# Optimization experiments

Hardware: AMD Instinct MI355X
Metric: run time of the kernel (lower is better)

## Reference

```python
import jax, jax.numpy as jnp
import numpy as np

NEAR_THRESHOLD = 0.25
N = 1536          # entities (== max_entities)
D = 768           # d_model
H = 64            # classifier hidden width
NTYPES = 4        # relation types: 0=NEAR, 1=APPROACHING, 2=FLEEING, 3=ABOVE
SPATIAL = 8       # geometric feature dim


def setup_inputs() -> dict:
    key = jax.random.key(0)
    ks = jax.random.split(key, 6)
    entity_embeddings = jax.random.normal(ks[0], (N, D), dtype=jnp.float32)
    positions = jax.random.uniform(ks[1], (N, 3), dtype=jnp.float32)
    prev_positions = jax.random.uniform(ks[2], (N, 3), dtype=jnp.float32)
    in_dim = 2 * D + SPATIAL
    W1 = jax.random.normal(ks[3], (in_dim, H), dtype=jnp.float32) * (1.0 / np.sqrt(in_dim))
    b1 = jnp.zeros((H,), dtype=jnp.float32)
    W2 = jax.random.normal(ks[4], (H, NTYPES), dtype=jnp.float32) * (1.0 / np.sqrt(H))
    b2 = jnp.zeros((NTYPES,), dtype=jnp.float32)
    return {"entity_embeddings": entity_embeddings, "positions": positions,
            "prev_positions": prev_positions, "W1": W1, "b1": b1, "W2": W2, "b2": b2}


def reference(entity_embeddings, positions, prev_positions, W1, b1, W2, b2):
    n, d = entity_embeddings.shape
    velocities = positions - prev_positions
    # pairwise geometry: entry [i, j] corresponds to pair (a=i, b=j)
    rel_pos = positions[None, :, :] - positions[:, None, :]      # (N, N, 3) = pos_b - pos_a
    rel_vel = velocities[None, :, :] - velocities[:, None, :]    # (N, N, 3)
    distance = jnp.linalg.norm(rel_pos, axis=-1)                 # (N, N)
    closing = -(rel_pos * rel_vel).sum(-1) / jnp.maximum(distance, 1e-6)
    vdiff = rel_pos[..., 1]
    # spatial feats = [dx, dy, dz, dist, dvx, dvy, dvz, vertical_diff]
    sp = jnp.concatenate([rel_pos, distance[..., None], rel_vel, vdiff[..., None]], axis=-1)  # (N, N, 8)

    # first Linear on concat([emb_a, emb_b, sp]) decomposed into three projections
    W1a, W1b, W1s = W1[:d], W1[d:2 * d], W1[2 * d:]
    ha = entity_embeddings @ W1a                                  # (N, H)
    hb = entity_embeddings @ W1b                                  # (N, H)
    hidden = jax.nn.relu(ha[:, None, :] + hb[None, :, :]
                         + jnp.einsum('ijs,sh->ijh', sp, W1s) + b1)  # (N, N, H)
    logits = hidden @ W2 + b2                                     # (N, N, 4)
    probs = jax.nn.softmax(logits, axis=-1)
    best_idx = jnp.argmax(probs, axis=-1)
    conf = jnp.max(probs, axis=-1)

    # conditional overrides (same priority order as _classify_pair)
    near = distance < NEAR_THRESHOLD
    appr = ~near & (closing > 0.05)
    flee = ~near & ~appr & (closing < -0.05)
    above = ~near & ~appr & ~flee & (jnp.abs(vdiff) > 0.3) & (distance < 0.5)
    rel_type = jnp.where(near, 0,
               jnp.where(appr, 1,
               jnp.where(flee, 2,
               jnp.where(above, 3, best_idx)))).astype(jnp.int32)
    conf_out = jnp.where(near, jnp.maximum(conf, 0.8),
               jnp.where(appr, jnp.maximum(conf, 0.6),
               jnp.where(flee, jnp.maximum(conf, 0.6),
               jnp.where(above, jnp.maximum(conf, 0.5), conf))))

    upper = jnp.triu(jnp.ones((n, n), dtype=bool), k=1)           # i < j pairs only
    valid = upper & (conf_out > 0.3)
    return rel_type, conf_out, valid
```

## Files before the change

kernel.cpp:

```cpp
#include <hip/hip_runtime.h>

typedef float f4 __attribute__((ext_vector_type(4)));

#define N 1536
#define D 768
#define H 64
#define NN (N * N)

__global__ __launch_bounds__(128) void k1_gemm(
    const float* __restrict__ E, const float* __restrict__ pos,
    const float* __restrict__ ppos, const float* __restrict__ W1,
    const float* __restrict__ b1, float* __restrict__ P, int KC)
{
    __shared__ float Es[8][192];

    const int tid = threadIdx.x;
    const int i0  = blockIdx.x * 8;
    const int kcc = blockIdx.y;
    const int k0  = kcc * KC;

    const int hg  = tid & 31;
    const int h0  = hg * 4;
    const int mat = h0 >> 6;
    const int hc  = h0 & 63;
    const int rp  = tid >> 5;
    const float* Wbase = W1 + (size_t)(mat * D + k0) * H + hc;

    f4 acc0 = {0.f, 0.f, 0.f, 0.f};
    f4 acc1 = {0.f, 0.f, 0.f, 0.f};

    for (int ks = 0; ks < KC; ks += 192) {
        if (ks) __syncthreads();
        for (int f = tid; f < 8 * 48; f += 128) {
            int row = f / 48, c = f - row * 48;
            *(f4*)&Es[row][c * 4] =
                *(const f4*)&E[(size_t)(i0 + row) * D + k0 + ks + c * 4];
        }
        __syncthreads();

        const float* Wc  = Wbase + (size_t)ks * H;
        const float* e0p = Es[2 * rp];
        const float* e1p = Es[2 * rp + 1];
        for (int kk = 0; kk < 192; kk += 8) {
#pragma unroll
            for (int u = 0; u < 8; ++u) {
                f4 w = *(const f4*)&Wc[(size_t)(kk + u) * H];
                float e0 = e0p[kk + u], e1 = e1p[kk + u];
                acc0 = __builtin_elementwise_fma((f4){e0, e0, e0, e0}, w, acc0);
                acc1 = __builtin_elementwise_fma((f4){e1, e1, e1, e1}, w, acc1);
            }
        }
    }

    if (kcc == 0) {
        const float* Ws = W1 + (size_t)2 * D * H + hc;
        f4 wp0 = *(const f4*)&Ws[0 * H];
        f4 wp1 = *(const f4*)&Ws[1 * H] + *(const f4*)&Ws[7 * H];
        f4 wp2 = *(const f4*)&Ws[2 * H];
        f4 wv0 = *(const f4*)&Ws[4 * H];
        f4 wv1 = *(const f4*)&Ws[5 * H];
        f4 wv2 = *(const f4*)&Ws[6 * H];
        f4 bb  = *(const f4*)&b1[hc];
#pragma unroll
        for (int r = 0; r < 2; ++r) {
            int i = i0 + 2 * rp + r;
            float px = pos[3 * i], py = pos[3 * i + 1], pz = pos[3 * i + 2];
            float vx = px - ppos[3 * i];
            float vy = py - ppos[3 * i + 1];
            float vz = pz - ppos[3 * i + 2];
            f4 g = px * wp0 + py * wp1 + pz * wp2 + vx * wv0 + vy * wv1 + vz * wv2;
            f4 add = (mat == 0) ? (bb - g) : g;
            if (r == 0) acc0 += add; else acc1 += add;
        }
    }

#pragma unroll
    for (int r = 0; r < 2; ++r) {
        int i = i0 + 2 * rp + r;
        f4 a = r ? acc1 : acc0;
#pragma unroll
        for (int c = 0; c < 4; ++c)
            P[(size_t)(kcc * 128 + h0 + c) * N + i] = a[c];
    }
}

__global__ __launch_bounds__(128) void k2_main(
    const float* __restrict__ P, int nkc,
    const float* __restrict__ W1, const float* __restrict__ W2,
    const float* __restrict__ b2, const float* __restrict__ pos,
    const float* __restrict__ ppos, float* __restrict__ out)
{
    __shared__ float As[64][32];
    __shared__ f4 Bs[64][16];
    __shared__ float w3s[64];
    __shared__ f4 W2s[64];
    __shared__ float pis[32][3], vis[32][3], pjs[64][3], vjs[64][3];

    const int tid = threadIdx.x;
    const int i0 = blockIdx.y * 32;
    const int j0 = blockIdx.x * 64;

#pragma unroll
    for (int g = 0; g < 4; ++g) {
        int f = g * 128 + tid;
        int h = f >> 3, c = f & 7;
        f4 s = {0.f, 0.f, 0.f, 0.f};
        for (int kc = 0; kc < nkc; ++kc)
            s += *(const f4*)&P[(size_t)(kc * 128 + h) * N + i0 + c * 4];
        *(f4*)&As[h][c * 4] = s;
    }
#pragma unroll
    for (int g = 0; g < 8; ++g) {
        int f = g * 128 + tid;
        int h = f >> 4, c = f & 15;
        f4 s = {0.f, 0.f, 0.f, 0.f};
        for (int kc = 0; kc < nkc; ++kc)
            s += *(const f4*)&P[(size_t)(kc * 128 + 64 + h) * N + j0 + c * 4];
        Bs[h][c] = s;
    }
    if (tid < 64) {
        w3s[tid] = W1[(size_t)(2 * D + 3) * H + tid];
        W2s[tid] = *(const f4*)&W2[tid * 4];
        int j = j0 + tid;
        float px = pos[3 * j], py = pos[3 * j + 1], pz = pos[3 * j + 2];
        pjs[tid][0] = px; pjs[tid][1] = py; pjs[tid][2] = pz;
        vjs[tid][0] = px - ppos[3 * j];
        vjs[tid][1] = py - ppos[3 * j + 1];
        vjs[tid][2] = pz - ppos[3 * j + 2];
    } else if (tid < 96) {
        int t = tid - 64;
        int i = i0 + t;
        float px = pos[3 * i], py = pos[3 * i + 1], pz = pos[3 * i + 2];
        pis[t][0] = px; pis[t][1] = py; pis[t][2] = pz;
        vis[t][0] = px - ppos[3 * i];
        vis[t][1] = py - ppos[3 * i + 1];
        vis[t][2] = pz - ppos[3 * i + 2];
    }
    __syncthreads();

    const int tx = tid & 15;
    const int ty = tid >> 4;

    float dist[4][4];
    {
#pragma clang fp contract(off)
#pragma unroll
        for (int a = 0; a < 4; ++a) {
#pragma unroll
            for (int b = 0; b < 4; ++b) {
                int il = ty * 4 + a, jl = tx * 4 + b;
                float dx = pjs[jl][0] - pis[il][0];
                float dy = pjs[jl][1] - pis[il][1];
                float dz = pjs[jl][2] - pis[il][2];
                float s = dx * dx;
                s = s + dy * dy;
                s = s + dz * dz;
                dist[a][b] = sqrtf(s);
            }
        }
    }

    f4 acc[4][4];
#pragma unroll
    for (int a = 0; a < 4; ++a)
#pragma unroll
        for (int b = 0; b < 4; ++b)
            acc[a][b] = (f4){0.f, 0.f, 0.f, 0.f};

#pragma unroll 4
    for (int h = 0; h < 64; ++h) {
        f4 A4 = *(const f4*)&As[h][ty * 4];
        f4 B4 = Bs[h][tx];
        float w3h = w3s[h];
        f4 w2r = W2s[h];
#pragma unroll
        for (int a = 0; a < 4; ++a) {
#pragma unroll
            for (int b = 0; b < 4; ++b) {
                float hid = fmaf(dist[a][b], w3h, A4[a] + B4[b]);
                hid = fmaxf(hid, 0.f);
                acc[a][b] = __builtin_elementwise_fma(
                    (f4){hid, hid, hid, hid}, w2r, acc[a][b]);
            }
        }
    }

    const f4 B2v = *(const f4*)b2;

#pragma unroll
    for (int a = 0; a < 4; ++a) {
        int il = ty * 4 + a;
        int i = i0 + il;
        f4 rt4, cf4, vl4;
#pragma unroll
        for (int b = 0; b < 4; ++b) {
            int jl = tx * 4 + b;
            int j = j0 + jl;
            float dd = dist[a][b];
            float dy, closing;
            {
#pragma clang fp contract(off)
                float dx = pjs[jl][0] - pis[il][0];
                dy       = pjs[jl][1] - pis[il][1];
                float dz = pjs[jl][2] - pis[il][2];
                float rvx = vjs[jl][0] - vis[il][0];
                float rvy = vjs[jl][1] - vis[il][1];
                float rvz = vjs[jl][2] - vis[il][2];
                float dot = dx * rvx;
                dot = dot + dy * rvy;
                dot = dot + dz * rvz;
                closing = -dot / fmaxf(dd, 1e-6f);
            }
            f4 l = acc[a][b] + B2v;
            float mx = l.x; int bidx = 0;
            if (l.y > mx) { mx = l.y; bidx = 1; }
            if (l.z > mx) { mx = l.z; bidx = 2; }
            if (l.w > mx) { mx = l.w; bidx = 3; }
            float s = expf(l.x - mx);
            s += expf(l.y - mx);
            s += expf(l.z - mx);
            s += expf(l.w - mx);
            float conf = 1.0f / s;

            bool near = dd < 0.25f;
            bool appr = !near && (closing > 0.05f);
            bool flee = !near && !appr && (closing < -0.05f);
            bool above = !near && !appr && !flee && (fabsf(dy) > 0.3f) && (dd < 0.5f);
            int rt = near ? 0 : appr ? 1 : flee ? 2 : above ? 3 : bidx;
            float co = near  ? fmaxf(conf, 0.8f)
                     : appr  ? fmaxf(conf, 0.6f)
                     : flee  ? fmaxf(conf, 0.6f)
                     : above ? fmaxf(conf, 0.5f)
                             : conf;
            float vd = ((j > i) && (co > 0.3f)) ? 1.0f : 0.0f;
            rt4[b] = (float)rt;
            cf4[b] = co;
            vl4[b] = vd;
        }
        int col = j0 + tx * 4;
        *(f4*)&out[(size_t)i * N + col]                  = rt4;
        *(f4*)&out[(size_t)NN + (size_t)i * N + col]     = cf4;
        *(f4*)&out[(size_t)2 * NN + (size_t)i * N + col] = vl4;
    }
}

extern "C" void kernel_launch(void* const* d_in, const int* in_sizes, int n_in,
                              void* d_out, int out_size, void* d_ws, size_t ws_size,
                              hipStream_t stream)
{
    const float* E    = (const float*)d_in[0];
    const float* pos  = (const float*)d_in[1];
    const float* ppos = (const float*)d_in[2];
    const float* W1   = (const float*)d_in[3];
    const float* b1   = (const float*)d_in[4];
    const float* W2   = (const float*)d_in[5];
    const float* b2   = (const float*)d_in[6];
    float* out = (float*)d_out;
    float* P   = (float*)d_ws;

    int nkc = (ws_size >= (size_t)4 * 128 * N * 4) ? 4 : 1;
    int KC  = D / nkc;

    dim3 g1(N / 8, nkc);
    k1_gemm<<<g1, 128, 0, stream>>>(E, pos, ppos, W1, b1, P, KC);

    dim3 g2(N / 64, N / 32);
    k2_main<<<g2, 128, 0, stream>>>(P, nkc, W1, W2, b2, pos, ppos, out);
}
```

Measured before the change: 150.3 us.

## Shrink pair tile to 32x32, pre-reduce K-split partials, packed f2 math

Adds a separate reduce kernel that sums the K-split partial projections once, so the main kernel no longer re-reads and sums the partials in every tile. The main kernel tile drops from 32x64 to 32x32 pairs per block, giving twice as many blocks and fewer accumulators per thread. Geometry (distance, dy, closing) is now computed up front and kept in registers, and shared memory for geometry and projections is overlaid with a union. The hidden-layer loop uses 2-wide packed FMA/max and reads W2 and w3 straight from global memory instead of shared. The cost is an extra launch, more workspace, and less reuse per block.

```diff
diff --git a/kernel.cpp b/kernel.cpp
--- a/kernel.cpp
+++ b/kernel.cpp
@@ -1,6 +1,7 @@
 #include <hip/hip_runtime.h>
 
 typedef float f4 __attribute__((ext_vector_type(4)));
+typedef float f2 __attribute__((ext_vector_type(2)));
 
 #define N 1536
 #define D 768
@@ -84,104 +85,114 @@
     }
 }
 
+__global__ __launch_bounds__(256) void k1b_reduce(
+    const float* __restrict__ P, float* __restrict__ AB, int nkc)
+{
+    int idx = blockIdx.x * 256 + threadIdx.x;
+    f4 s = {0.f, 0.f, 0.f, 0.f};
+    for (int kc = 0; kc < nkc; ++kc)
+        s += *(const f4*)&P[(size_t)kc * 128 * N + (size_t)idx * 4];
+    *(f4*)&AB[(size_t)idx * 4] = s;
+}
+
 __global__ __launch_bounds__(128) void k2_main(
-    const float* __restrict__ P, int nkc,
-    const float* __restrict__ W1, const float* __restrict__ W2,
-    const float* __restrict__ b2, const float* __restrict__ pos,
-    const float* __restrict__ ppos, float* __restrict__ out)
-{
-    __shared__ float As[64][32];
-    __shared__ f4 Bs[64][16];
-    __shared__ float w3s[64];
-    __shared__ f4 W2s[64];
-    __shared__ float pis[32][3], vis[32][3], pjs[64][3], vjs[64][3];
+    const float* __restrict__ AB, const float* __restrict__ W1,
+    const float* __restrict__ W2, const float* __restrict__ b2,
+    const float* __restrict__ pos, const float* __restrict__ ppos,
+    float* __restrict__ out)
+{
+    __shared__ union SMem {
+        struct { float pi[32][3], vi[32][3], pj[32][3], vj[32][3]; } g;
+        struct { float As[64][32], Bs[64][32]; } t;
+    } sm;
 
     const int tid = threadIdx.x;
     const int i0 = blockIdx.y * 32;
-    const int j0 = blockIdx.x * 64;
+    const int j0 = blockIdx.x * 32;
+
+    if (tid < 32) {
+        int i = i0 + tid;
+        float px = pos[3 * i], py = pos[3 * i + 1], pz = pos[3 * i + 2];
+        sm.g.pi[tid][0] = px; sm.g.pi[tid][1] = py; sm.g.pi[tid][2] = pz;
+        sm.g.vi[tid][0] = px - ppos[3 * i];
+        sm.g.vi[tid][1] = py - ppos[3 * i + 1];
+        sm.g.vi[tid][2] = pz - ppos[3 * i + 2];
+    } else if (tid < 64) {
+        int t = tid - 32;
+        int j = j0 + t;
+        float px = pos[3 * j], py = pos[3 * j + 1], pz = pos[3 * j + 2];
+        sm.g.pj[t][0] = px; sm.g.pj[t][1] = py; sm.g.pj[t][2] = pz;
+        sm.g.vj[t][0] = px - ppos[3 * j];
+        sm.g.vj[t][1] = py - ppos[3 * j + 1];
+        sm.g.vj[t][2] = pz - ppos[3 * j + 2];
+    }
+    __syncthreads();
+
+    const int tx = tid & 15;
+    const int ty = tid >> 4;
+
+    f2 dd[4], dyv[4], clv[4];
+    {
+#pragma clang fp contract(off)
+#pragma unroll
+        for (int a = 0; a < 4; ++a) {
+#pragma unroll
+            for (int b = 0; b < 2; ++b) {
+                int il = ty * 4 + a, jl = tx * 2 + b;
+                float dx = sm.g.pj[jl][0] - sm.g.pi[il][0];
+                float dy = sm.g.pj[jl][1] - sm.g.pi[il][1];
+                float dz = sm.g.pj[jl][2] - sm.g.pi[il][2];
+                float s = dx * dx;
+                s = s + dy * dy;
+                s = s + dz * dz;
+                float d = sqrtf(s);
+                float rvx = sm.g.vj[jl][0] - sm.g.vi[il][0];
+                float rvy = sm.g.vj[jl][1] - sm.g.vi[il][1];
+                float rvz = sm.g.vj[jl][2] - sm.g.vi[il][2];
+                float dot = dx * rvx;
+                dot = dot + dy * rvy;
+                dot = dot + dz * rvz;
+                float cl = -dot / fmaxf(d, 1e-6f);
+                dd[a][b] = d; dyv[a][b] = dy; clv[a][b] = cl;
+            }
+        }
+    }
+    __syncthreads();
 
 #pragma unroll
     for (int g = 0; g < 4; ++g) {
         int f = g * 128 + tid;
         int h = f >> 3, c = f & 7;
-        f4 s = {0.f, 0.f, 0.f, 0.f};
-        for (int kc = 0; kc < nkc; ++kc)
-            s += *(const f4*)&P[(size_t)(kc * 128 + h) * N + i0 + c * 4];
-        *(f4*)&As[h][c * 4] = s;
-    }
-#pragma unroll
-    for (int g = 0; g < 8; ++g) {
-        int f = g * 128 + tid;
-        int h = f >> 4, c = f & 15;
-        f4 s = {0.f, 0.f, 0.f, 0.f};
-        for (int kc = 0; kc < nkc; ++kc)
-            s += *(const f4*)&P[(size_t)(kc * 128 + 64 + h) * N + j0 + c * 4];
-        Bs[h][c] = s;
-    }
-    if (tid < 64) {
-        w3s[tid] = W1[(size_t)(2 * D + 3) * H + tid];
-        W2s[tid] = *(const f4*)&W2[tid * 4];
-        int j = j0 + tid;
-        float px = pos[3 * j], py = pos[3 * j + 1], pz = pos[3 * j + 2];
-        pjs[tid][0] = px; pjs[tid][1] = py; pjs[tid][2] = pz;
-        vjs[tid][0] = px - ppos[3 * j];
-        vjs[tid][1] = py - ppos[3 * j + 1];
-        vjs[tid][2] = pz - ppos[3 * j + 2];
-    } else if (tid < 96) {
-        int t = tid - 64;
-        int i = i0 + t;
-        float px = pos[3 * i], py = pos[3 * i + 1], pz = pos[3 * i + 2];
-        pis[t][0] = px; pis[t][1] = py; pis[t][2] = pz;
-        vis[t][0] = px - ppos[3 * i];
-        vis[t][1] = py - ppos[3 * i + 1];
-        vis[t][2] = pz - ppos[3 * i + 2];
+        *(f4*)&sm.t.As[h][c * 4] = *(const f4*)&AB[(size_t)h * N + i0 + c * 4];
+        *(f4*)&sm.t.Bs[h][c * 4] = *(const f4*)&AB[(size_t)(64 + h) * N + j0 + c * 4];
     }
     __syncthreads();
 
-    const int tx = tid & 15;
-    const int ty = tid >> 4;
-
-    float dist[4][4];
-    {
-#pragma clang fp contract(off)
-#pragma unroll
-        for (int a = 0; a < 4; ++a) {
-#pragma unroll
-            for (int b = 0; b < 4; ++b) {
-                int il = ty * 4 + a, jl = tx * 4 + b;
-                float dx = pjs[jl][0] - pis[il][0];
-                float dy = pjs[jl][1] - pis[il][1];
-                float dz = pjs[jl][2] - pis[il][2];
-                float s = dx * dx;
-                s = s + dy * dy;
-                s = s + dz * dz;
-                dist[a][b] = sqrtf(s);
-            }
-        }
-    }
-
-    f4 acc[4][4];
+    f2 acc[4][4];
 #pragma unroll
     for (int a = 0; a < 4; ++a)
 #pragma unroll
-        for (int b = 0; b < 4; ++b)
-            acc[a][b] = (f4){0.f, 0.f, 0.f, 0.f};
+        for (int l = 0; l < 4; ++l)
+            acc[a][l] = (f2){0.f, 0.f};
+
+    const float* w3p = W1 + (size_t)(2 * D + 3) * H;
 
 #pragma unroll 4
     for (int h = 0; h < 64; ++h) {
-        f4 A4 = *(const f4*)&As[h][ty * 4];
-        f4 B4 = Bs[h][tx];
-        float w3h = w3s[h];
-        f4 w2r = W2s[h];
+        f4 A4 = *(const f4*)&sm.t.As[h][ty * 4];
+        f2 B2 = *(const f2*)&sm.t.Bs[h][tx * 2];
+        float w3h = w3p[h];
+        f4 w2r = *(const f4*)&W2[h * 4];
+        f2 w3v = (f2){w3h, w3h};
 #pragma unroll
         for (int a = 0; a < 4; ++a) {
-#pragma unroll
-            for (int b = 0; b < 4; ++b) {
-                float hid = fmaf(dist[a][b], w3h, A4[a] + B4[b]);
-                hid = fmaxf(hid, 0.f);
-                acc[a][b] = __builtin_elementwise_fma(
-                    (f4){hid, hid, hid, hid}, w2r, acc[a][b]);
-            }
+            f2 pre = (f2){A4[a], A4[a]} + B2;
+            f2 hid = __builtin_elementwise_fma(dd[a], w3v, pre);
+            hid = __builtin_elementwise_max(hid, (f2){0.f, 0.f});
+            acc[a][0] = __builtin_elementwise_fma(hid, (f2){w2r.x, w2r.x}, acc[a][0]);
+            acc[a][1] = __builtin_elementwise_fma(hid, (f2){w2r.y, w2r.y}, acc[a][1]);
+            acc[a][2] = __builtin_elementwise_fma(hid, (f2){w2r.z, w2r.z}, acc[a][2]);
+            acc[a][3] = __builtin_elementwise_fma(hid, (f2){w2r.w, w2r.w}, acc[a][3]);
         }
     }
 
@@ -189,43 +200,32 @@
 
 #pragma unroll
     for (int a = 0; a < 4; ++a) {
-        int il = ty * 4 + a;
-        int i = i0 + il;
-        f4 rt4, cf4, vl4;
-#pragma unroll
-        for (int b = 0; b < 4; ++b) {
-            int jl = tx * 4 + b;
-            int j = j0 + jl;
-            float dd = dist[a][b];
-            float dy, closing;
-            {
-#pragma clang fp contract(off)
-                float dx = pjs[jl][0] - pis[il][0];
-                dy       = pjs[jl][1] - pis[il][1];
-                float dz = pjs[jl][2] - pis[il][2];
-                float rvx = vjs[jl][0] - vis[il][0];
-                float rvy = vjs[jl][1] - vis[il][1];
-                float rvz = vjs[jl][2] - vis[il][2];
-                float dot = dx * rvx;
-                dot = dot + dy * rvy;
-                dot = dot + dz * rvz;
-                closing = -dot / fmaxf(dd, 1e-6f);
-            }
-            f4 l = acc[a][b] + B2v;
-            float mx = l.x; int bidx = 0;
-            if (l.y > mx) { mx = l.y; bidx = 1; }
-            if (l.z > mx) { mx = l.z; bidx = 2; }
-            if (l.w > mx) { mx = l.w; bidx = 3; }
-            float s = expf(l.x - mx);
-            s += expf(l.y - mx);
-            s += expf(l.z - mx);
-            s += expf(l.w - mx);
+        int i = i0 + ty * 4 + a;
+        f2 rt2, cf2, vl2;
+#pragma unroll
+        for (int b = 0; b < 2; ++b) {
+            int j = j0 + tx * 2 + b;
+            float l0 = acc[a][0][b] + B2v.x;
+            float l1 = acc[a][1][b] + B2v.y;
+            float l2 = acc[a][2][b] + B2v.z;
+            float l3 = acc[a][3][b] + B2v.w;
+            float mx = l0; int bidx = 0;
+            if (l1 > mx) { mx = l1; bidx = 1; }
+            if (l2 > mx) { mx = l2; bidx = 2; }
+            if (l3 > mx) { mx = l3; bidx = 3; }
+            float s = expf(l0 - mx);
+            s += expf(l1 - mx);
+            s += expf(l2 - mx);
+            s += expf(l3 - mx);
             float conf = 1.0f / s;
 
-            bool near = dd < 0.25f;
-            bool appr = !near && (closing > 0.05f);
-            bool flee = !near && !appr && (closing < -0.05f);
-            bool above = !near && !appr && !flee && (fabsf(dy) > 0.3f) && (dd < 0.5f);
+            float d  = dd[a][b];
+            float dy = dyv[a][b];
+            float cl = clv[a][b];
+            bool near = d < 0.25f;
+            bool appr = !near && (cl > 0.05f);
+            bool flee = !near && !appr && (cl < -0.05f);
+            bool above = !near && !appr && !flee && (fabsf(dy) > 0.3f) && (d < 0.5f);
             int rt = near ? 0 : appr ? 1 : flee ? 2 : above ? 3 : bidx;
             float co = near  ? fmaxf(conf, 0.8f)
                      : appr  ? fmaxf(conf, 0.6f)
@@ -233,14 +233,14 @@
                      : above ? fmaxf(conf, 0.5f)
                              : conf;
             float vd = ((j > i) && (co > 0.3f)) ? 1.0f : 0.0f;
-            rt4[b] = (float)rt;
-            cf4[b] = co;
-            vl4[b] = vd;
-        }
-        int col = j0 + tx * 4;
-        *(f4*)&out[(size_t)i * N + col]                  = rt4;
-        *(f4*)&out[(size_t)NN + (size_t)i * N + col]     = cf4;
-        *(f4*)&out[(size_t)2 * NN + (size_t)i * N + col] = vl4;
+            rt2[b] = (float)rt;
+            cf2[b] = co;
+            vl2[b] = vd;
+        }
+        int col = j0 + tx * 2;
+        *(f2*)&out[(size_t)i * N + col]                  = rt2;
+        *(f2*)&out[(size_t)NN + (size_t)i * N + col]     = cf2;
+        *(f2*)&out[(size_t)2 * NN + (size_t)i * N + col] = vl2;
     }
 }
 
@@ -258,12 +258,23 @@
     float* out = (float*)d_out;
     float* P   = (float*)d_ws;
 
-    int nkc = (ws_size >= (size_t)4 * 128 * N * 4) ? 4 : 1;
+    const size_t part_sz = (size_t)4 * 128 * N;
+    const size_t ab_sz   = (size_t)128 * N;
+    int nkc = (ws_size >= (part_sz + ab_sz) * sizeof(float)) ? 4 : 1;
     int KC  = D / nkc;
 
     dim3 g1(N / 8, nkc);
     k1_gemm<<<g1, 128, 0, stream>>>(E, pos, ppos, W1, b1, P, KC);
 
-    dim3 g2(N / 64, N / 32);
-    k2_main<<<g2, 128, 0, stream>>>(P, nkc, W1, W2, b2, pos, ppos, out);
-}
+    const float* AB;
+    if (nkc > 1) {
+        float* ABw = P + part_sz;
+        k1b_reduce<<<(128 * N / 4) / 256, 256, 0, stream>>>(P, ABw, nkc);
+        AB = ABw;
+    } else {
+        AB = P;
+    }
+
+    dim3 g2(N / 32, N / 32);
+    k2_main<<<g2, 128, 0, stream>>>(AB, W1, W2, b2, pos, ppos, out);
+}
```

Result: faster. 123.4 us (-17.9%).
